# Optimization experiments

Measured on AMD Instinct MI355X. Metric: run time of the kernel, lower is better.

## Reference

```python
import jax, jax.numpy as jnp
import numpy as np

B = 524288       # batch
N_QUBITS = 16    # data dimension == wires
LAYERS = 8
N_READOUT = 2    # PauliZ on wires (0, 1)


def setup_inputs() -> dict:
    key = jax.random.key(0)
    k1, k2, k3 = jax.random.split(key, 3)
    X = jax.random.uniform(k1, (B, N_QUBITS), dtype=jnp.float32)
    params = 0.01 * jax.random.normal(k2, (LAYERS, N_QUBITS, 3), dtype=jnp.float32)
    head_w = jax.random.normal(k3, (1, N_READOUT), dtype=jnp.float32) / jnp.sqrt(float(N_READOUT))
    head_b = jnp.zeros((1,), dtype=jnp.float32)
    return {"X": X, "params": params, "head_w": head_w, "head_b": head_b}


def _rot_matrix(phi, theta, omega):
    """PennyLane qml.Rot(phi, theta, omega) = RZ(omega) RY(theta) RZ(phi); [Q,2,2] complex."""
    ct = jnp.cos(theta * 0.5)
    st = jnp.sin(theta * 0.5)
    m00 = jnp.exp(-0.5j * (phi + omega)) * ct
    m01 = -jnp.exp(0.5j * (phi - omega)) * st
    m10 = jnp.exp(-0.5j * (phi - omega)) * st
    m11 = jnp.exp(0.5j * (phi + omega)) * ct
    return jnp.stack([jnp.stack([m00, m01], axis=-1),
                      jnp.stack([m10, m11], axis=-1)], axis=-2)


def reference(X, params, head_w, head_b):
    # No entanglement (default) -> circuit is a product of single-qubit circuits;
    # simulate per-(batch, qubit) 2-amplitude states, fully batched.
    half = X * 0.5
    # AngleEmbedding (RX per wire) applied to |0>: (cos(x/2), -i sin(x/2))
    state = jnp.stack([jnp.cos(half) + 0j, -1j * jnp.sin(half)], axis=-1)  # [B,Q,2] c64
    for l in range(params.shape[0]):
        M = _rot_matrix(params[l, :, 0], params[l, :, 1], params[l, :, 2])  # [Q,2,2]
        state = jnp.einsum('qij,bqj->bqi', M, state)
    probs = state.real ** 2 + state.imag ** 2            # [B,Q,2]
    ez = probs[..., 0] - probs[..., 1]                   # <Z> per wire, [B,Q]
    E = ez[:, :N_READOUT]                                # readout wires (0, 1)
    logits = E @ head_w.T + head_b                       # [B,1]
    return logits.squeeze(-1)
```

## Files before the change

kernel.cpp:

```cpp
#include <hip/hip_runtime.h>
#include <math.h>

#define NQ 16
#define LAYERS 8

__global__ __launch_bounds__(64) void vqc_prep(
        const float* __restrict__ params,
        const float* __restrict__ head_w,
        const float* __restrict__ head_b,
        float* __restrict__ coef)
{
    __shared__ float sM[2][LAYERS][8];
    __shared__ float sP[2][3];

    int tid = threadIdx.x;
    if (tid < 16) {
        int q = tid >> 3;
        int l = tid & 7;
        float phi = params[(l * NQ + q) * 3 + 0];
        float th  = params[(l * NQ + q) * 3 + 1];
        float om  = params[(l * NQ + q) * 3 + 2];
        float ct, st, c_p, s_p, c_m, s_m;
        __sincosf(0.5f * th, &st, &ct);
        __sincosf(-0.5f * (phi + om), &s_p, &c_p);
        __sincosf( 0.5f * (phi - om), &s_m, &c_m);
        float* M = sM[q][l];
        M[0] =  c_p * ct;  M[1] =  s_p * ct;
        M[2] = -c_m * st;  M[3] = -s_m * st;
        M[4] =  c_m * st;  M[5] = -s_m * st;
        M[6] =  c_p * ct;  M[7] = -s_p * ct;
    }
    __syncthreads();

    if (tid < 2) {
        int q = tid;
        float u00r = 1.f, u00i = 0.f, u01r = 0.f, u01i = 0.f;
        float u10r = 0.f, u10i = 0.f, u11r = 1.f, u11i = 0.f;
        for (int l = 0; l < LAYERS; ++l) {
            const float* M = sM[q][l];
            float m00r = M[0], m00i = M[1], m01r = M[2], m01i = M[3];
            float m10r = M[4], m10i = M[5], m11r = M[6], m11i = M[7];
            float n00r = m00r*u00r - m00i*u00i + m01r*u10r - m01i*u10i;
            float n00i = m00r*u00i + m00i*u00r + m01r*u10i + m01i*u10r;
            float n01r = m00r*u01r - m00i*u01i + m01r*u11r - m01i*u11i;
            float n01i = m00r*u01i + m00i*u01r + m01r*u11i + m01i*u11r;
            float n10r = m10r*u00r - m10i*u00i + m11r*u10r - m11i*u10i;
            float n10i = m10r*u00i + m10i*u00r + m11r*u10i + m11i*u10r;
            float n11r = m10r*u01r - m10i*u01i + m11r*u11r - m11i*u11i;
            float n11i = m10r*u01i + m10i*u01r + m11r*u11i + m11i*u11r;
            u00r = n00r; u00i = n00i; u01r = n01r; u01i = n01i;
            u10r = n10r; u10i = n10i; u11r = n11r; u11i = n11i;
        }
        float d0 = (u00r*u00r + u00i*u00i) - (u10r*u10r + u10i*u10i);
        float d1 = (u01r*u01r + u01i*u01i) - (u11r*u11r + u11i*u11i);
        float A  = 0.5f * (d0 + d1);
        float Bc = 0.5f * (d0 - d1);
        float im0 = u00i*u01r - u00r*u01i;
        float im1 = u10i*u11r - u10r*u11i;
        float Bs = -(im0 - im1);
        float w = head_w[q];
        sP[q][0] = w * A;
        sP[q][1] = w * Bc;
        sP[q][2] = w * Bs;
    }
    __syncthreads();

    if (tid == 0) {
        coef[0] = head_b[0] + sP[0][0] + sP[1][0];
        coef[1] = sP[0][1];
        coef[2] = sP[0][2];
        coef[3] = sP[1][1];
        coef[4] = sP[1][2];
    }
}

__global__ __launch_bounds__(256) void vqc_main(const float* __restrict__ X,
                                                const float* __restrict__ coef,
                                                float* __restrict__ out,
                                                int n)
{
    int b = blockIdx.x * blockDim.x + threadIdx.x;
    if (b >= n) return;
    float C  = coef[0];
    float K0 = coef[1], K1 = coef[2], K2 = coef[3], K3 = coef[4];
    float2 x = *(const float2*)(X + (size_t)b * NQ);
    float s0, c0, s1, c1;
    __sincosf(x.x, &s0, &c0);
    __sincosf(x.y, &s1, &c1);
    out[b] = C + K0 * c0 + K1 * s0 + K2 * c1 + K3 * s1;
}

extern "C" void kernel_launch(void* const* d_in, const int* in_sizes, int n_in,
                              void* d_out, int out_size, void* d_ws, size_t ws_size,
                              hipStream_t stream) {
    const float* X      = (const float*)d_in[0];
    const float* params = (const float*)d_in[1];
    const float* head_w = (const float*)d_in[2];
    const float* head_b = (const float*)d_in[3];
    float* out  = (float*)d_out;
    float* coef = (float*)d_ws;

    vqc_prep<<<1, 64, 0, stream>>>(params, head_w, head_b, coef);

    int threads = 256;
    int blocks  = (out_size + threads - 1) / threads;
    vqc_main<<<blocks, threads, 0, stream>>>(X, coef, out, out_size);
}
```

Measured before the change: 79.07 us.

## Fuse coefficient prep into main kernel using shuffle-based matrix product tree

Removes the separate single-block prep kernel and its launch and serialization by having every block recompute the per-wire unitary products. The eight layer matrices are combined with an xor-shuffle reduction tree across lanes instead of a serial loop, and the readout coefficients go into shared memory. The X load is issued before the prep work so its latency overlaps. In exchange, every block repeats the params loads, trig and matrix work and adds a __syncthreads before its output.

Result: no change. 78.67 us (-0.5%).

```diff
diff --git a/kernel.cpp b/kernel.cpp
--- a/kernel.cpp
+++ b/kernel.cpp
@@ -4,16 +4,48 @@
 #define NQ 16
 #define LAYERS 8
 
-__global__ __launch_bounds__(64) void vqc_prep(
+struct M22 {
+    float r00, i00, r01, i01, r10, i10, r11, i11;
+};
+
+__device__ __forceinline__ M22 cmul(const M22& A, const M22& B) {
+    M22 p;
+    p.r00 = A.r00*B.r00 - A.i00*B.i00 + A.r01*B.r10 - A.i01*B.i10;
+    p.i00 = A.r00*B.i00 + A.i00*B.r00 + A.r01*B.i10 + A.i01*B.r10;
+    p.r01 = A.r00*B.r01 - A.i00*B.i01 + A.r01*B.r11 - A.i01*B.i11;
+    p.i01 = A.r00*B.i01 + A.i00*B.r01 + A.r01*B.i11 + A.i01*B.r11;
+    p.r10 = A.r10*B.r00 - A.i10*B.i00 + A.r11*B.r10 - A.i11*B.i10;
+    p.i10 = A.r10*B.i00 + A.i10*B.r00 + A.r11*B.i10 + A.i11*B.r10;
+    p.r11 = A.r10*B.r01 - A.i10*B.i01 + A.r11*B.r11 - A.i11*B.i11;
+    p.i11 = A.r10*B.i01 + A.i10*B.r01 + A.r11*B.i11 + A.i11*B.r11;
+    return p;
+}
+
+__device__ __forceinline__ M22 mshfl_xor(const M22& A, int mask) {
+    M22 p;
+    p.r00 = __shfl_xor(A.r00, mask); p.i00 = __shfl_xor(A.i00, mask);
+    p.r01 = __shfl_xor(A.r01, mask); p.i01 = __shfl_xor(A.i01, mask);
+    p.r10 = __shfl_xor(A.r10, mask); p.i10 = __shfl_xor(A.i10, mask);
+    p.r11 = __shfl_xor(A.r11, mask); p.i11 = __shfl_xor(A.i11, mask);
+    return p;
+}
+
+__global__ __launch_bounds__(256) void vqc_fused(
+        const float* __restrict__ X,
         const float* __restrict__ params,
         const float* __restrict__ head_w,
         const float* __restrict__ head_b,
-        float* __restrict__ coef)
+        float* __restrict__ out,
+        int n)
 {
-    __shared__ float sM[2][LAYERS][8];
-    __shared__ float sP[2][3];
+    __shared__ float sC[6];
 
     int tid = threadIdx.x;
+    int b = blockIdx.x * blockDim.x + tid;
+
+    float2 x = make_float2(0.f, 0.f);
+    if (b < n) x = *(const float2*)(X + (size_t)b * NQ);
+
     if (tid < 16) {
         int q = tid >> 3;
         int l = tid & 7;
@@ -24,66 +56,40 @@
         __sincosf(0.5f * th, &st, &ct);
         __sincosf(-0.5f * (phi + om), &s_p, &c_p);
         __sincosf( 0.5f * (phi - om), &s_m, &c_m);
-        float* M = sM[q][l];
-        M[0] =  c_p * ct;  M[1] =  s_p * ct;
-        M[2] = -c_m * st;  M[3] = -s_m * st;
-        M[4] =  c_m * st;  M[5] = -s_m * st;
-        M[6] =  c_p * ct;  M[7] = -s_p * ct;
+        M22 U;
+        U.r00 =  c_p * ct;  U.i00 =  s_p * ct;
+        U.r01 = -c_m * st;  U.i01 = -s_m * st;
+        U.r10 =  c_m * st;  U.i10 = -s_m * st;
+        U.r11 =  c_p * ct;  U.i11 = -s_p * ct;
+
+        #pragma unroll
+        for (int mask = 1; mask <= 4; mask <<= 1) {
+            M22 other = mshfl_xor(U, mask);
+            bool upper = (tid & mask) != 0;
+            M22 left  = upper ? U : other;
+            M22 right = upper ? other : U;
+            U = cmul(left, right);
+        }
+
+        if (l == 0) {
+            float d0 = (U.r00*U.r00 + U.i00*U.i00) - (U.r10*U.r10 + U.i10*U.i10);
+            float d1 = (U.r01*U.r01 + U.i01*U.i01) - (U.r11*U.r11 + U.i11*U.i11);
+            float A  = 0.5f * (d0 + d1);
+            float Bc = 0.5f * (d0 - d1);
+            float im0 = U.i00*U.r01 - U.r00*U.i01;
+            float im1 = U.i10*U.r11 - U.r10*U.i11;
+            float Bs = -(im0 - im1);
+            float w = head_w[q];
+            sC[3*q + 0] = w * A;
+            sC[3*q + 1] = w * Bc;
+            sC[3*q + 2] = w * Bs;
+        }
     }
     __syncthreads();
 
-    if (tid < 2) {
-        int q = tid;
-        float u00r = 1.f, u00i = 0.f, u01r = 0.f, u01i = 0.f;
-        float u10r = 0.f, u10i = 0.f, u11r = 1.f, u11i = 0.f;
-        for (int l = 0; l < LAYERS; ++l) {
-            const float* M = sM[q][l];
-            float m00r = M[0], m00i = M[1], m01r = M[2], m01i = M[3];
-            float m10r = M[4], m10i = M[5], m11r = M[6], m11i = M[7];
-            float n00r = m00r*u00r - m00i*u00i + m01r*u10r - m01i*u10i;
-            float n00i = m00r*u00i + m00i*u00r + m01r*u10i + m01i*u10r;
-            float n01r = m00r*u01r - m00i*u01i + m01r*u11r - m01i*u11i;
-            float n01i = m00r*u01i + m00i*u01r + m01r*u11i + m01i*u11r;
-            float n10r = m10r*u00r - m10i*u00i + m11r*u10r - m11i*u10i;
-            float n10i = m10r*u00i + m10i*u00r + m11r*u10i + m11i*u10r;
-            float n11r = m10r*u01r - m10i*u01i + m11r*u11r - m11i*u11i;
-            float n11i = m10r*u01i + m10i*u01r + m11r*u11i + m11i*u11r;
-            u00r = n00r; u00i = n00i; u01r = n01r; u01i = n01i;
-            u10r = n10r; u10i = n10i; u11r = n11r; u11i = n11i;
-        }
-        float d0 = (u00r*u00r + u00i*u00i) - (u10r*u10r + u10i*u10i);
-        float d1 = (u01r*u01r + u01i*u01i) - (u11r*u11r + u11i*u11i);
-        float A  = 0.5f * (d0 + d1);
-        float Bc = 0.5f * (d0 - d1);
-        float im0 = u00i*u01r - u00r*u01i;
-        float im1 = u10i*u11r - u10r*u11i;
-        float Bs = -(im0 - im1);
-        float w = head_w[q];
-        sP[q][0] = w * A;
-        sP[q][1] = w * Bc;
-        sP[q][2] = w * Bs;
-    }
-    __syncthreads();
-
-    if (tid == 0) {
-        coef[0] = head_b[0] + sP[0][0] + sP[1][0];
-        coef[1] = sP[0][1];
-        coef[2] = sP[0][2];
-        coef[3] = sP[1][1];
-        coef[4] = sP[1][2];
-    }
-}
-
-__global__ __launch_bounds__(256) void vqc_main(const float* __restrict__ X,
-                                                const float* __restrict__ coef,
-                                                float* __restrict__ out,
-                                                int n)
-{
-    int b = blockIdx.x * blockDim.x + threadIdx.x;
     if (b >= n) return;
-    float C  = coef[0];
-    float K0 = coef[1], K1 = coef[2], K2 = coef[3], K3 = coef[4];
-    float2 x = *(const float2*)(X + (size_t)b * NQ);
+    float C  = head_b[0] + sC[0] + sC[3];
+    float K0 = sC[1], K1 = sC[2], K2 = sC[4], K3 = sC[5];
     float s0, c0, s1, c1;
     __sincosf(x.x, &s0, &c0);
     __sincosf(x.y, &s1, &c1);
@@ -97,12 +103,9 @@
     const float* params = (const float*)d_in[1];
     const float* head_w = (const float*)d_in[2];
     const float* head_b = (const float*)d_in[3];
-    float* out  = (float*)d_out;
-    float* coef = (float*)d_ws;
-
-    vqc_prep<<<1, 64, 0, stream>>>(params, head_w, head_b, coef);
+    float* out = (float*)d_out;
 
     int threads = 256;
     int blocks  = (out_size + threads - 1) / threads;
-    vqc_main<<<blocks, threads, 0, stream>>>(X, coef, out, out_size);
+    vqc_fused<<<blocks, threads, 0, stream>>>(X, params, head_w, head_b, out, out_size);
 }
```
